# Kernel optimization log

Measured on AMD Instinct MI355X. Metric: run time of the kernel, lower is better.

The kernel has to match this reference:

```python
import jax, jax.numpy as jnp
import numpy as np
from jax.ops import segment_sum

N_NODES = 50000
N_EDGES = 400000
D_IN = 128
HIDDEN = [128, 128]
D_OUT = 64
ALPHA = 0.5


def _glorot(key, shape):
    fan_in, fan_out = shape
    lim = jnp.sqrt(6.0 / (fan_in + fan_out))
    return jax.random.uniform(key, shape, jnp.float32, -lim, lim)


def setup_inputs() -> dict:
    key = jax.random.key(0)
    ks = jax.random.split(key, 16)
    x = jax.random.normal(ks[0], (N_NODES, D_IN), jnp.float32)
    edge_index = jax.random.randint(ks[1], (2, N_EDGES), 0, N_NODES, jnp.int64)
    theta = jax.random.uniform(ks[2], (N_EDGES,), jnp.float32)
    return {
        "x": x,
        "edge_index": edge_index,
        "theta": theta,
        "W1_s2d": _glorot(ks[3], (D_IN, HIDDEN[0])),
        "W1_d2s": _glorot(ks[4], (D_IN, HIDDEN[0])),
        "b1_s2d": jnp.zeros((HIDDEN[0],), jnp.float32),
        "b1_d2s": jnp.zeros((HIDDEN[0],), jnp.float32),
        "W2_s2d": _glorot(ks[5], (HIDDEN[0], HIDDEN[1])),
        "W2_d2s": _glorot(ks[6], (HIDDEN[0], HIDDEN[1])),
        "b2_s2d": jnp.zeros((HIDDEN[1],), jnp.float32),
        "b2_d2s": jnp.zeros((HIDDEN[1],), jnp.float32),
        "W_ro": _glorot(ks[7], (HIDDEN[1], D_OUT)),
        "b_ro": jnp.zeros((D_OUT,), jnp.float32),
    }


def _fuzzy_laplacian(edge_index, theta, num_nodes):
    # bidirectional duplication + self loops (self_loop=True, edge_weight=1)
    senders, receivers = edge_index[0], edge_index[1]
    loop = jnp.arange(num_nodes, dtype=senders.dtype)
    cs = jnp.concatenate((senders, receivers, loop))
    cr = jnp.concatenate((receivers, senders, loop))
    c2, s2 = jnp.cos(theta) ** 2, jnp.sin(theta) ** 2
    ones = jnp.ones((num_nodes,), theta.dtype)
    # real(e^{i t})^2 = cos^2 t ; exp(i(pi/2 - t)) -> real^2 = sin^2 t
    out_w = jnp.concatenate((c2, s2, ones))
    in_w = jnp.concatenate((s2, c2, ones))
    deg_s = segment_sum(out_w, cs, num_segments=num_nodes) + 1e-12
    deg_r = segment_sum(in_w, cs, num_segments=num_nodes) + 1e-12
    dis_s = jnp.where(deg_s > 1e11, 0.0, jax.lax.rsqrt(deg_s))
    dis_r = jnp.where(deg_r > 1e11, 0.0, jax.lax.rsqrt(deg_r))
    w_s2d = dis_s[cs] * out_w * dis_r[cr]
    w_d2s = dis_r[cs] * in_w * dis_s[cr]
    return cs, cr, w_s2d, w_d2s


def _forward(x, edge_index, theta, W1_s2d, W1_d2s, b1_s2d, b1_d2s,
             W2_s2d, W2_d2s, b2_s2d, b2_d2s, W_ro, b_ro):
    num_nodes = x.shape[0]
    cs, cr, w_s2d, w_d2s = _fuzzy_laplacian(edge_index, theta, num_nodes)
    layers = [(W1_s2d, W1_d2s, b1_s2d, b1_d2s), (W2_s2d, W2_d2s, b2_s2d, b2_d2s)]
    for Ws, Wd, bs, bd in layers:
        xs = x[cs]  # [2E+N, F] gather
        agg_s = segment_sum(xs * w_s2d[:, None], cr, num_segments=num_nodes)
        agg_d = segment_sum(xs * w_d2s[:, None], cr, num_segments=num_nodes)
        x = ALPHA * (agg_s @ Ws + bs) + (1.0 - ALPHA) * (agg_d @ Wd + bd)
        x = jax.nn.relu(x)
    return x @ W_ro + b_ro


def reference(x, edge_index, theta, W1_s2d, W1_d2s, b1_s2d, b1_d2s,
              W2_s2d, W2_d2s, b2_s2d, b2_d2s, W_ro, b_ro):
    return _forward(x, edge_index, theta, W1_s2d, W1_d2s, b1_s2d, b1_d2s,
                    W2_s2d, W2_d2s, b2_s2d, b2_d2s, W_ro, b_ro)
```

## Files before the change

kernel.cpp:

```cpp
#include <hip/hip_runtime.h>
#include <hip/hip_fp16.h>

#define N_NODES 50000
#define N_EDGES 400000
#define CSR_E (2 * N_EDGES + N_NODES)
#define NCH 10
#define CHW 5000
#define NE2 (N_NODES * NCH)

typedef unsigned short ushort_t;
typedef unsigned int uint_t;
typedef __attribute__((ext_vector_type(8))) short bf16x8;
typedef __attribute__((ext_vector_type(4))) float f32x4;

__device__ __forceinline__ float bf2f(ushort_t u) {
    return __uint_as_float(((uint_t)u) << 16);
}
__device__ __forceinline__ ushort_t f2bf(float f) {
    uint_t b = __float_as_uint(f);
    b += 0x7FFFu + ((b >> 16) & 1u);
    return (ushort_t)(b >> 16);
}
__device__ __forceinline__ uint_t packw(float a, float b) {
    return ((uint_t)__half_as_ushort(__float2half(b)) << 16) |
           (uint_t)__half_as_ushort(__float2half(a));
}
__device__ __forceinline__ float unpl(uint_t w) {
    return __half2float(__ushort_as_half((ushort_t)(w & 0xffffu)));
}
__device__ __forceinline__ float unph(uint_t w) {
    return __half2float(__ushort_as_half((ushort_t)(w >> 16)));
}


__device__ int g_est;
__device__ int g_is16;
__device__ __align__(8) float2 g_dis2[N_NODES];
__device__ int g_cnt2[NE2];
__device__ int g_offs2[NE2 + 1];
__device__ uint_t g_rank[N_EDGES];
__device__ int g_bsum[512];
__device__ __align__(16) uint4 g_estage[N_EDGES];
__device__ __align__(16) uint2 g_csr8[CSR_E];
__device__ __align__(16) ushort_t g_h1[(size_t)N_NODES * 128];
__device__ __align__(16) ushort_t g_xcvt[(size_t)N_NODES * 128];
__device__ __align__(16) ushort_t g_bp1[8 * 128 * 32];
__device__ __align__(16) ushort_t g_bp2[8 * 128 * 32];
__device__ __align__(16) ushort_t g_bp3[4 * 64 * 32];
__device__ float g_bc1[128];
__device__ float g_bc2[128];
__device__ float g_bro[64];


__global__ __launch_bounds__(256) void init_all(const uint_t* __restrict__ xw,
                                                const int* __restrict__ eidx,
                                                const float* __restrict__ x32) {
    __shared__ int s_flags;
    if (threadIdx.x < 64) {
        uint_t w = xw[threadIdx.x];
        int elo = (w >> 7) & 0xFF;
        unsigned long long mb = __ballot(elo >= 100 && elo <= 150);
        unsigned long long me = __ballot(eidx[2 * threadIdx.x + 1] != 0);
        if (threadIdx.x == 0) {
            int is16 = (__popcll(mb) >= 48) ? 1 : 0;
            int est = me ? 1 : 2;
            s_flags = is16 | (est << 1);
        }
    }
    __syncthreads();
    int is16 = s_flags & 1;
    int t = blockIdx.x * 256 + threadIdx.x;
    if (t == 0) {
        g_is16 = is16;
        g_est = s_flags >> 1;
    }
    if (t < N_NODES) {
        int sc = t / CHW;
#pragma unroll
        for (int c = 0; c < NCH; c++) g_cnt2[t * NCH + c] = (c == sc) ? 1 : 0;
    }
    if (!is16 && t < N_NODES * 128 / 8) {
        const float4* p = (const float4*)(x32 + t * 8);
        float4 a = p[0], b = p[1];
        ushort4 o0, o1;
        o0.x = f2bf(a.x); o0.y = f2bf(a.y); o0.z = f2bf(a.z); o0.w = f2bf(a.w);
        o1.x = f2bf(b.x); o1.y = f2bf(b.y); o1.z = f2bf(b.z); o1.w = f2bf(b.w);
        *(ushort4*)(g_xcvt + t * 8) = o0;
        *(ushort4*)(g_xcvt + t * 8 + 4) = o1;
    }
}


__global__ __launch_bounds__(256) void edge_cnt(const int* __restrict__ eidx,
                                                const ushort_t* __restrict__ th16,
                                                const float* __restrict__ th32) {
    int e = blockIdx.x * 256 + threadIdx.x;
    if (e >= N_EDGES) return;
    int st = g_est;
    int s = eidx[(size_t)e * st];
    int r = eidx[((size_t)N_EDGES + e) * st];
    float t = g_is16 ? bf2f(th16[e]) : th32[e];
    float sn, cs_;
    sincosf(t, &sn, &cs_);
    float c2 = cs_ * cs_;
    float s2 = sn * sn;
    g_estage[e] = make_uint4((uint_t)s, (uint_t)r, __float_as_uint(c2), __float_as_uint(s2));
    int rf = atomicAdd(&g_cnt2[r * NCH + s / CHW], 1);
    int rr = atomicAdd(&g_cnt2[s * NCH + r / CHW], 1);
    g_rank[e] = (uint_t)rf | ((uint_t)rr << 16);
}


__global__ __launch_bounds__(1024) void scan1() {
    __shared__ int sd[1024];
    int i = blockIdx.x * 1024 + threadIdx.x;
    int v = (i < NE2) ? g_cnt2[i] : 0;
    sd[threadIdx.x] = v;
    __syncthreads();
    for (int o = 1; o < 1024; o <<= 1) {
        int tv = (threadIdx.x >= o) ? sd[threadIdx.x - o] : 0;
        __syncthreads();
        sd[threadIdx.x] += tv;
        __syncthreads();
    }
    if (i < NE2) g_offs2[i] = sd[threadIdx.x] - v;
    if (threadIdx.x == 1023) g_bsum[blockIdx.x] = sd[1023];
}


__global__ __launch_bounds__(256) void scan23() {
    __shared__ int sd[256];
    int b = blockIdx.x;
    int acc = 0;
    for (int j = (int)threadIdx.x; j < b; j += 256) acc += g_bsum[j];
    sd[threadIdx.x] = acc;
    __syncthreads();
#pragma unroll
    for (int o = 128; o > 0; o >>= 1) {
        if ((int)threadIdx.x < o) sd[threadIdx.x] += sd[threadIdx.x + o];
        __syncthreads();
    }
    int base = sd[0];
    int i0 = b << 10;
#pragma unroll
    for (int u = 0; u < 4; u++) {
        int i = i0 + u * 256 + threadIdx.x;
        if (i < NE2) g_offs2[i] += base;
    }
    if (b == 0 && threadIdx.x == 0) g_offs2[NE2] = CSR_E;
}


__global__ __launch_bounds__(256) void fill_all() {
    int e = blockIdx.x * 256 + threadIdx.x;
    if (e < N_EDGES) {
        uint4 stg = g_estage[e];
        int s = (int)stg.x;
        int r = (int)stg.y;
        float c2 = __uint_as_float(stg.z);
        float s2 = __uint_as_float(stg.w);
        uint_t rk = g_rank[e];
        int pf = g_offs2[r * NCH + s / CHW] + (int)(rk & 0xffffu);
        int pr = g_offs2[s * NCH + r / CHW] + (int)(rk >> 16);
        g_csr8[pf] = make_uint2((uint_t)s, packw(c2, s2));
        g_csr8[pr] = make_uint2((uint_t)r, packw(s2, c2));
    }
    if (e < N_NODES) {
        g_csr8[g_offs2[e * NCH + e / CHW]] = make_uint2((uint_t)e, packw(1.0f, 1.0f));
    }
}


__global__ __launch_bounds__(256) void deg_pass() {
    int n = blockIdx.x * 256 + threadIdx.x;
    if (n >= N_NODES) return;
    int kb = g_offs2[n * NCH];
    int ke = g_offs2[n * NCH + NCH];
    float ds = 0.f, dr = 0.f;
    for (int k = kb; k < ke; k++) {
        uint_t w = g_csr8[k].y;
        ds += unph(w);
        dr += unpl(w);
    }
    g_dis2[n] = make_float2(rsqrtf(ds + 1e-12f), rsqrtf(dr + 1e-12f));
}


__global__ __launch_bounds__(256) void finalize_w() {
    int i = blockIdx.x * 256 + threadIdx.x;
    if (i >= CSR_E) return;
    uint2 e = g_csr8[i];
    float2 d = g_dis2[e.x];
    ((uint_t*)g_csr8)[2 * (size_t)i + 1] = packw(d.x * unpl(e.y), d.y * unph(e.y));
}


__global__ __launch_bounds__(256) void prep_all(const ushort_t* W1s16, const float* W1s32,
                                                const ushort_t* W1d16, const float* W1d32,
                                                const ushort_t* b1s16, const float* b1s32,
                                                const ushort_t* b1d16, const float* b1d32,
                                                const ushort_t* W2s16, const float* W2s32,
                                                const ushort_t* W2d16, const float* W2d32,
                                                const ushort_t* b2s16, const float* b2s32,
                                                const ushort_t* b2d16, const float* b2d32,
                                                const ushort_t* Wro16, const float* Wro32,
                                                const ushort_t* bro16, const float* bro32) {
    int is16 = g_is16;
    int t = blockIdx.x * 256 + threadIdx.x;
    if (t < 2 * 32768) {
        int layer = t >> 15;
        int i = t & 32767;
        const ushort_t* Ws16 = layer ? W2s16 : W1s16;
        const float* Ws32 = layer ? W2s32 : W1s32;
        const ushort_t* Wd16 = layer ? W2d16 : W1d16;
        const float* Wd32 = layer ? W2d32 : W1d32;
        ushort_t* Bp = layer ? g_bp2 : g_bp1;
        int k = i >> 7, n = i & 127;
        ushort_t v;
        if (k < 128) {
            int idx = k * 128 + n;
            v = is16 ? Ws16[idx] : f2bf(Ws32[idx]);
        } else {
            int idx = (k - 128) * 128 + n;
            v = is16 ? Wd16[idx] : f2bf(Wd32[idx]);
        }
        int kb = k >> 5, kk = k & 31;
        Bp[((kb * 128 + n) << 5) + kk] = v;
        if (i < 128) {
            const ushort_t* bs16 = layer ? b2s16 : b1s16;
            const float* bs32 = layer ? b2s32 : b1s32;
            const ushort_t* bd16 = layer ? b2d16 : b1d16;
            const float* bd32 = layer ? b2d32 : b1d32;
            float a = is16 ? bf2f(bs16[i]) : bs32[i];
            float b = is16 ? bf2f(bd16[i]) : bd32[i];
            (layer ? g_bc2 : g_bc1)[i] = 0.5f * (a + b);
        }
    } else if (t < 2 * 32768 + 8192) {
        int i = t - 2 * 32768;
        int k = i >> 6, n = i & 63;
        ushort_t v = is16 ? Wro16[i] : f2bf(Wro32[i]);
        int kb = k >> 5, kk = k & 31;
        g_bp3[((kb * 64 + n) << 5) + kk] = v;
        if (i < 64) g_bro[i] = is16 ? bf2f(bro16[i]) : bro32[i];
    }
}


template <int LAYER>
__global__ __launch_bounds__(256) void fused_layer(const ushort_t* __restrict__ xext,
                                                   void* __restrict__ outp) {
    __shared__ ushort_t tA[16 * 256];
    __shared__ ushort_t tH[(LAYER == 1) ? 16 * 128 : 1];
    int w = threadIdx.x >> 6;
    int lane = threadIdx.x & 63;
    int gsel = lane >> 4;
    int r = lane & 15;
    int lrow = w * 4 + gsel;
    int node = blockIdx.x * 16 + lrow;
    const ushort_t* xin = (LAYER == 0) ? (g_is16 ? xext : g_xcvt) : g_h1;

    int ks = g_offs2[node * NCH];
    int ke = g_offs2[node * NCH + NCH];
    int c0 = ke - ks;
    int cmax = c0;
    cmax = max(cmax, __shfl_xor(cmax, 16));
    cmax = max(cmax, __shfl_xor(cmax, 32));

    float accS[8], accD[8];
#pragma unroll
    for (int f = 0; f < 8; f++) { accS[f] = 0.f; accD[f] = 0.f; }

    uint2 ecur = g_csr8[ks + min(r, c0 - 1)];
    int lbase = lane & 48;
    for (int k = 0; k < cmax; k += 16) {
        uint2 enext = ecur;
        if (k + 16 < cmax) enext = g_csr8[ks + min(k + 16 + r, c0 - 1)];
        int jend = cmax - k;
#pragma unroll
        for (int j = 0; j < 16; j++) {
            if (j >= jend) break;
            uint_t ex = (uint_t)__shfl((int)ecur.x, lbase | j, 64);
            uint_t ey = (uint_t)__shfl((int)ecur.y, lbase | j, 64);
            bf16x8 v = *(const bf16x8*)(xin + (size_t)ex * 128 + r * 8);
            bool val = (k + j) < c0;
            float ws_ = val ? unpl(ey) : 0.f;
            float wd_ = val ? unph(ey) : 0.f;
#pragma unroll
            for (int f = 0; f < 8; f++) {
                float xv = bf2f((ushort_t)v[f]);
                accS[f] = fmaf(ws_, xv, accS[f]);
                accD[f] = fmaf(wd_, xv, accD[f]);
            }
        }
        ecur = enext;
    }

    float2 dn = g_dis2[node];
    float fs = 0.5f * dn.y;
    float fd = 0.5f * dn.x;
    uint_t oS[4], oD[4];
#pragma unroll
    for (int p = 0; p < 4; p++) {
        oS[p] = ((uint_t)f2bf(accS[2 * p + 1] * fs) << 16) | (uint_t)f2bf(accS[2 * p] * fs);
        oD[p] = ((uint_t)f2bf(accD[2 * p + 1] * fd) << 16) | (uint_t)f2bf(accD[2 * p] * fd);
    }
    int swA = (lrow & 7) << 4;
    *(uint4*)((char*)tA + ((lrow * 512 + r * 16) ^ swA)) = make_uint4(oS[0], oS[1], oS[2], oS[3]);
    *(uint4*)((char*)tA + ((lrow * 512 + 256 + r * 16) ^ swA)) = make_uint4(oD[0], oD[1], oD[2], oD[3]);
    __syncthreads();

    int cc = lane & 15;
    int q = lane >> 4;
    int csw = (cc & 7) << 4;
    const ushort_t* Bp = (LAYER == 0) ? g_bp1 : g_bp2;
    const float* bias = (LAYER == 0) ? g_bc1 : g_bc2;
    f32x4 acc0 = {0.f, 0.f, 0.f, 0.f};
    f32x4 acc1 = {0.f, 0.f, 0.f, 0.f};
#pragma unroll
    for (int kb = 0; kb < 8; kb++) {
        bf16x8 a = *(const bf16x8*)((const char*)tA + ((cc * 512 + kb * 64 + q * 16) ^ csw));
        bf16x8 b0 = *(const bf16x8*)(Bp + (((kb * 128 + w * 32 + cc) << 5) + q * 8));
        bf16x8 b1 = *(const bf16x8*)(Bp + (((kb * 128 + w * 32 + 16 + cc) << 5) + q * 8));
        acc0 = __builtin_amdgcn_mfma_f32_16x16x32_bf16(a, b0, acc0, 0, 0, 0);
        acc1 = __builtin_amdgcn_mfma_f32_16x16x32_bf16(a, b1, acc1, 0, 0, 0);
    }
    int mb = blockIdx.x * 16;
    float bi0 = bias[w * 32 + cc];
    float bi1 = bias[w * 32 + 16 + cc];
    if (LAYER == 0) {
#pragma unroll
        for (int rr = 0; rr < 4; rr++) {
            int m = mb + q * 4 + rr;
            g_h1[(size_t)m * 128 + w * 32 + cc] = f2bf(fmaxf(acc0[rr] + bi0, 0.f));
            g_h1[(size_t)m * 128 + w * 32 + 16 + cc] = f2bf(fmaxf(acc1[rr] + bi1, 0.f));
        }
    } else {
#pragma unroll
        for (int rr = 0; rr < 4; rr++) {
            int ml = q * 4 + rr;
            int msw = (ml & 7) << 4;
            *(ushort_t*)((char*)tH + ((ml * 256 + (w * 32 + cc) * 2) ^ msw)) =
                f2bf(fmaxf(acc0[rr] + bi0, 0.f));
            *(ushort_t*)((char*)tH + ((ml * 256 + (w * 32 + 16 + cc) * 2) ^ msw)) =
                f2bf(fmaxf(acc1[rr] + bi1, 0.f));
        }
        __syncthreads();
        f32x4 a3 = {0.f, 0.f, 0.f, 0.f};
#pragma unroll
        for (int kb = 0; kb < 4; kb++) {
            bf16x8 a = *(const bf16x8*)((const char*)tH + ((cc * 256 + kb * 64 + q * 16) ^ csw));
            bf16x8 b = *(const bf16x8*)(g_bp3 + (((kb * 64 + w * 16 + cc) << 5) + q * 8));
            a3 = __builtin_amdgcn_mfma_f32_16x16x32_bf16(a, b, a3, 0, 0, 0);
        }
        int is16 = g_is16;
        float bi = g_bro[w * 16 + cc];
#pragma unroll
        for (int rr = 0; rr < 4; rr++) {
            int m = mb + q * 4 + rr;
            float v = a3[rr] + bi;
            if (is16)
                ((ushort_t*)outp)[(size_t)m * 64 + w * 16 + cc] = f2bf(v);
            else
                ((float*)outp)[(size_t)m * 64 + w * 16 + cc] = v;
        }
    }
}


static inline int cdiv(int a, int b) { return (a + b - 1) / b; }

extern "C" void kernel_launch(void* const* d_in, const int* in_sizes, int n_in,
                              void* d_out, int out_size, void* d_ws, size_t ws_size,
                              hipStream_t stream) {
    const void* x = d_in[0];
    const int* eidx = (const int*)d_in[1];
    const void* theta = d_in[2];
    const void* W1s = d_in[3];
    const void* W1d = d_in[4];
    const void* b1s = d_in[5];
    const void* b1d = d_in[6];
    const void* W2s = d_in[7];
    const void* W2d = d_in[8];
    const void* b2s = d_in[9];
    const void* b2d = d_in[10];
    const void* Wro = d_in[11];
    const void* bro = d_in[12];
    (void)in_sizes; (void)n_in; (void)out_size; (void)d_ws; (void)ws_size;

    const int NB2 = cdiv(NE2, 1024);

    init_all<<<cdiv(N_NODES * 128 / 8, 256), 256, 0, stream>>>(
        (const uint_t*)x, eidx, (const float*)x);
    edge_cnt<<<cdiv(N_EDGES, 256), 256, 0, stream>>>(
        eidx, (const ushort_t*)theta, (const float*)theta);
    scan1<<<NB2, 1024, 0, stream>>>();
    scan23<<<NB2, 256, 0, stream>>>();
    fill_all<<<cdiv(N_EDGES, 256), 256, 0, stream>>>();
    deg_pass<<<cdiv(N_NODES, 256), 256, 0, stream>>>();
    finalize_w<<<cdiv(CSR_E, 256), 256, 0, stream>>>();
    prep_all<<<cdiv(2 * 32768 + 8192, 256), 256, 0, stream>>>(
        (const ushort_t*)W1s, (const float*)W1s, (const ushort_t*)W1d, (const float*)W1d,
        (const ushort_t*)b1s, (const float*)b1s, (const ushort_t*)b1d, (const float*)b1d,
        (const ushort_t*)W2s, (const float*)W2s, (const ushort_t*)W2d, (const float*)W2d,
        (const ushort_t*)b2s, (const float*)b2s, (const ushort_t*)b2d, (const float*)b2d,
        (const ushort_t*)Wro, (const float*)Wro, (const ushort_t*)bro, (const float*)bro);

    const int AB = N_NODES / 16;
    fused_layer<0><<<AB, 256, 0, stream>>>((const ushort_t*)x, nullptr);
    fused_layer<1><<<AB, 256, 0, stream>>>(nullptr, d_out);
}
```

Measured before the change: 272.1 us.

## Batch gathered row loads in groups of eight and remap blocks across XCDs

The edge aggregation loop now issues eight independent row gathers before consuming them, instead of loading and accumulating one edge at a time. This raises memory-level parallelism for the bf16 feature gathers but always runs all 16 slots, with zero weights for padding. Block IDs are also remapped so consecutive node tiles land on the same XCD, which is meant to improve L2 locality. The remap assumes exactly 3125 blocks (5*391+3*390); duplicated edge indices clamp to valid addresses, and more registers are held live.

```diff
diff --git a/kernel.cpp b/kernel.cpp
--- a/kernel.cpp
+++ b/kernel.cpp
@@ -256,7 +256,13 @@
     int gsel = lane >> 4;
     int r = lane & 15;
     int lrow = w * 4 + gsel;
-    int node = blockIdx.x * 16 + lrow;
+
+    int bid = blockIdx.x;
+    int xcd = bid & 7;
+    int idx = bid >> 3;
+    int nbid = (xcd < 5 ? xcd * 391 : 5 * 391 + (xcd - 5) * 390) + idx;
+
+    int node = nbid * 16 + lrow;
     const ushort_t* xin = (LAYER == 0) ? (g_is16 ? xext : g_xcvt) : g_h1;
 
     int ks = g_offs2[node * NCH];
@@ -275,21 +281,29 @@
     for (int k = 0; k < cmax; k += 16) {
         uint2 enext = ecur;
         if (k + 16 < cmax) enext = g_csr8[ks + min(k + 16 + r, c0 - 1)];
-        int jend = cmax - k;
-#pragma unroll
-        for (int j = 0; j < 16; j++) {
-            if (j >= jend) break;
-            uint_t ex = (uint_t)__shfl((int)ecur.x, lbase | j, 64);
-            uint_t ey = (uint_t)__shfl((int)ecur.y, lbase | j, 64);
-            bf16x8 v = *(const bf16x8*)(xin + (size_t)ex * 128 + r * 8);
-            bool val = (k + j) < c0;
-            float ws_ = val ? unpl(ey) : 0.f;
-            float wd_ = val ? unph(ey) : 0.f;
-#pragma unroll
-            for (int f = 0; f < 8; f++) {
-                float xv = bf2f((ushort_t)v[f]);
-                accS[f] = fmaf(ws_, xv, accS[f]);
-                accD[f] = fmaf(wd_, xv, accD[f]);
+#pragma unroll
+        for (int h = 0; h < 2; h++) {
+            uint_t eys[8];
+            bf16x8 vs[8];
+#pragma unroll
+            for (int j = 0; j < 8; j++) {
+                int jj = h * 8 + j;
+                uint_t ex = (uint_t)__shfl((int)ecur.x, lbase | jj, 64);
+                eys[j] = (uint_t)__shfl((int)ecur.y, lbase | jj, 64);
+                vs[j] = *(const bf16x8*)(xin + (size_t)ex * 128 + r * 8);
+            }
+#pragma unroll
+            for (int j = 0; j < 8; j++) {
+                int jj = h * 8 + j;
+                bool val = (k + jj) < c0;
+                float ws_ = val ? unpl(eys[j]) : 0.f;
+                float wd_ = val ? unph(eys[j]) : 0.f;
+#pragma unroll
+                for (int f = 0; f < 8; f++) {
+                    float xv = bf2f((ushort_t)vs[j][f]);
+                    accS[f] = fmaf(ws_, xv, accS[f]);
+                    accD[f] = fmaf(wd_, xv, accD[f]);
+                }
             }
         }
         ecur = enext;
@@ -324,7 +338,7 @@
         acc0 = __builtin_amdgcn_mfma_f32_16x16x32_bf16(a, b0, acc0, 0, 0, 0);
         acc1 = __builtin_amdgcn_mfma_f32_16x16x32_bf16(a, b1, acc1, 0, 0, 0);
     }
-    int mb = blockIdx.x * 16;
+    int mb = nbid * 16;
     float bi0 = bias[w * 32 + cc];
     float bi1 = bias[w * 32 + 16 + cc];
     if (LAYER == 0) {
```

Measured after the change: 269.7 us. No clear change (-0.9%).
